# Kernel optimization log

Hardware: AMD Instinct MI355X
Metric: run time of the kernel (lower is better)

Reference implementation:

```python
import jax, jax.numpy as jnp
import numpy as np

# Static config (matches init_kwargs)
B, F, CIN, COUT, H, W = 2, 8, 16, 32, 128, 128
RB, GB = 1, 1                 # refer_band, guard_band_dop (range_doppler)
KH, KW = 2 * (RB + GB), 4     # PeakConv kernel
N = KH * KW                   # ring samples per pixel (16)
LEAK, EPS = 0.01, 1e-5


def _ring_offsets(rb, gb):
    """Peripheral-reference-frame ring offsets, in the exact order of _gen_prf_grid."""
    r = rb + gb
    hp = 2 * r + 1
    xs, ys = np.meshgrid(np.arange(-r, r + 1), np.arange(-r, r + 1), indexing='ij')
    def ring(a):
        top = a[0:rb]
        rgt = a[rb:hp - 2 * rb + 1, hp - rb:hp]
        dwn = a[hp - rb:hp]
        lft = a[rb:hp - 2 * rb + 1, 0:rb]
        return np.concatenate([top.ravel(), rgt.ravel(), dwn.ravel(), lft.ravel()])
    return ring(xs), ring(ys)

_OX, _OY = _ring_offsets(RB, GB)  # each (N,)


def _peak_conv(x, Wk, bk):
    # x: (b, c, h, w)
    bsz, c, h, w = x.shape
    pad = RB + GB
    xp = jnp.pad(x, ((0, 0), (0, 0), (pad, pad), (pad, pad)))
    ii = jnp.arange(h)[:, None, None] + pad + jnp.asarray(_OX)[None, None, :]  # (h,1,N)
    jj = jnp.arange(w)[None, :, None] + pad + jnp.asarray(_OY)[None, None, :]  # (1,w,N)
    x_r = xp[:, :, ii, jj]                       # (b,c,h,w,N) ring gather
    diff = x[..., None] - x_r                    # center minus ring (x_c - x_r)
    diff = diff.reshape(bsz, c, h, w, KH, KW)    # matches _reshape_x_prf tiling
    # conv with kernel (KH,KW), stride (KH,KW) over tiled map == per-pixel contraction
    return jnp.einsum('bchwgj,ocgj->bohw', diff, Wk) + bk[None, :, None, None]


def _bn_leaky(x, gamma, beta):
    mu = x.mean(axis=(0, 2, 3), keepdims=True)
    var = x.var(axis=(0, 2, 3), keepdims=True)  # biased, as torch BN uses for normalization
    y = (x - mu) * jax.lax.rsqrt(var + EPS)
    y = y * gamma[None, :, None, None] + beta[None, :, None, None]
    return jnp.where(y >= 0, y, LEAK * y)


def setup_inputs() -> dict:
    key = jax.random.key(0)
    ks = jax.random.split(key, 5)
    return {
        'x':  jax.random.normal(ks[0], (B, CIN, F, H, W), dtype=jnp.float32),
        'W1': jax.random.normal(ks[1], (COUT, CIN, KH, KW), dtype=jnp.float32) * 0.05,
        'b1': jax.random.normal(ks[2], (COUT,), dtype=jnp.float32) * 0.05,
        'g1': jnp.ones((COUT,), jnp.float32),
        'be1': jnp.zeros((COUT,), jnp.float32),
        'W2': jax.random.normal(ks[3], (COUT, COUT, KH, KW), dtype=jnp.float32) * 0.05,
        'b2': jax.random.normal(ks[4], (COUT,), dtype=jnp.float32) * 0.05,
        'g2': jnp.ones((COUT,), jnp.float32),
        'be2': jnp.zeros((COUT,), jnp.float32),
    }


def reference(x, W1, b1, g1, be1, W2, b2, g2, be2):
    # (B, CIN, F, H, W) -> permute -> flatten to (B*F, CIN, H, W)
    xx = jnp.transpose(x, (0, 2, 1, 3, 4)).reshape(B * F, CIN, H, W)
    y = _bn_leaky(_peak_conv(xx, W1, b1), g1, be1)
    y = _bn_leaky(_peak_conv(y, W2, b2), g2, be2)
    # NOTE: original does .view(B, C, F, h, w) on a (B*F, C, h, w) contiguous
    # tensor — a raw reinterpretation, reproduced exactly by this reshape.
    y = y.reshape(B, COUT, F, H, W)
    return y.mean(axis=2, keepdims=True)  # AvgPool3d((F,1,1)) -> (B, COUT, 1, H, W)
```

## Files before the change

### kernel.cpp

```cpp
#include <hip/hip_runtime.h>
#include <hip/hip_bf16.h>

using short8 = __attribute__((ext_vector_type(8))) short;
using sh4    = __attribute__((ext_vector_type(4))) short;
using f32x4  = __attribute__((ext_vector_type(4))) float;
typedef unsigned short ushort_t;
typedef unsigned long long u64;

constexpr int BB = 2, FF = 8, CIN = 16, COUT = 32, HH = 128, WW = 128;
constexpr int HW   = HH * WW;
constexpr int NIMG = BB * FF;
constexpr int TIL = 16, HALO = 2, LP = 20, NPX = 400;
constexpr int WFN = 17 * 2 * 512;
constexpr int NCPY = 64;
constexpr float FXS  = 65536.f;
constexpr float IFXS = 1.f / 65536.f;

__device__ const int DOFF[17] = { -42,-41,-40,-39,-38, -18,2,22, 38,39,40,41,42, -22,-2,18, 0 };

__device__ __forceinline__ float leaky(float v) { return fmaxf(v, 0.01f * v); }
__device__ __forceinline__ ushort_t f2bf(float f) {
    return __builtin_bit_cast(ushort_t, __float2bfloat16(f));
}
__device__ __forceinline__ float bf2f(ushort_t h) {
    unsigned u = ((unsigned)h) << 16;
    return __builtin_bit_cast(float, u);
}

__device__ __forceinline__ void prm_from_acc(const u64* __restrict__ acc,
                                             const float* __restrict__ gamma,
                                             const float* __restrict__ beta,
                                             float* sprm, int tid)
{
    if (tid < COUT) {
        long long ls = 0, lq = 0;
#pragma unroll
        for (int k = 0; k < NCPY; ++k) {
            ls += (long long)acc[k * 64 + tid];
            lq += (long long)acc[k * 64 + COUT + tid];
        }
        float s = (float)ls * IFXS;
        float q = (float)lq * IFXS;
        const float n = (float)(NIMG * HW);
        float mu  = s / n;
        float var = q / n - mu * mu;
        float a   = gamma[tid] * rsqrtf(var + 1e-5f);
        sprm[tid]        = a;
        sprm[COUT + tid] = beta[tid] - mu * a;
    }
    __syncthreads();
}

template <int MODE>
__device__ __forceinline__ void conv_phase(
    const float* __restrict__ inf, const ushort_t* __restrict__ inh,
    const ushort_t* __restrict__ Wf, const float* __restrict__ bk,
    const float* sprm, ushort_t* __restrict__ tout, u64* __restrict__ acc_g,
    ushort_t* lds, float (*redS)[COUT], float (*redQ)[COUT],
    int img, int tileid, int tid)
{
    const int tx   = (tileid & 7) * TIL;
    const int ty   = (tileid >> 3) * TIL;
    const int lane = tid & 63;
    const int wid  = tid >> 6;
    const int rxl  = lane & 15;
    const int cq   = lane >> 4;

    if (MODE == 0) {
#pragma unroll
        for (int e = 0; e < 4; ++e) {
            int task = e * 256 + tid;
            if (task < 800) {
                int h  = task >= 400 ? 1 : 0;
                int p  = task - h * 400;
                int ry = p / LP, rx = p - ry * LP;
                int gh = ty + ry - HALO, gw = tx + rx - HALO;
                bool ok = (unsigned)gh < (unsigned)HH && (unsigned)gw < (unsigned)WW;
                int ghc = min(max(gh, 0), HH - 1), gwc = min(max(gw, 0), WW - 1);
                const float* base = inf + (((size_t)(img >> 3) * CIN + 8 * h) * FF + (img & 7)) * HW
                                       + ghc * WW + gwc;
                short8 hi8, lo8;
#pragma unroll
                for (int cc = 0; cc < 8; ++cc) {
                    float v = base[(size_t)cc * FF * HW];
                    v = ok ? v : 0.f;
                    ushort_t hi = f2bf(v);
                    hi8[cc] = (short)hi;
                    lo8[cc] = (short)f2bf(v - bf2f(hi));
                }
                int swz = (p & 3) ^ ((p >> 2) & 3);
                *(short8*)&lds[p * 32 + 8 * (h ^ swz)]       = hi8;
                *(short8*)&lds[p * 32 + 8 * ((2 + h) ^ swz)] = lo8;
            }
        }
    } else {
#pragma unroll
        for (int e = 0; e < 7; ++e) {
            int task = e * 256 + tid;
            if (task < 1600) {
                int g  = task & 3, p = task >> 2;
                int ry = p / LP, rx = p - ry * LP;
                int gh = ty + ry - HALO, gw = tx + rx - HALO;
                bool ok = (unsigned)gh < (unsigned)HH && (unsigned)gw < (unsigned)WW;
                int ghc = min(max(gh, 0), HH - 1), gwc = min(max(gw, 0), WW - 1);
                const ushort_t* px = inh + ((size_t)img * HW + ghc * WW + gwc) * 32 + 8 * g;
                short8 raw = *(const short8*)px;
                short8 hv;
#pragma unroll
                for (int jj = 0; jj < 8; ++jj) {
                    int c = 8 * g + jj;
                    float v = bf2f((ushort_t)raw[jj]);
                    v = leaky(fmaf(sprm[c], v, sprm[COUT + c]));
                    hv[jj] = (short)f2bf(ok ? v : 0.f);
                }
                int swz = (p & 3) ^ ((p >> 2) & 3);
                *(short8*)&lds[p * 32 + 8 * (g ^ swz)] = hv;
            }
        }
    }
    __syncthreads();

    f32x4 acc[4][2];
#pragma unroll
    for (int ng = 0; ng < 4; ++ng)
#pragma unroll
        for (int oh = 0; oh < 2; ++oh) acc[ng][oh] = f32x4{0.f, 0.f, 0.f, 0.f};

    int q0[4];
#pragma unroll
    for (int ng = 0; ng < 4; ++ng) q0[ng] = (wid * 4 + ng + HALO) * LP + (rxl + HALO);

    const ushort_t* wl = Wf + (size_t)lane * 8;

#pragma unroll
    for (int n = 0; n < 17; ++n) {
        short8 A0 = *(const short8*)(wl + (size_t)(n * 2 + 0) * 512);
        short8 A1 = *(const short8*)(wl + (size_t)(n * 2 + 1) * 512);
        int dof = DOFF[n];
#pragma unroll
        for (int ng = 0; ng < 4; ++ng) {
            int p   = q0[ng] + dof;
            int swz = (p & 3) ^ ((p >> 2) & 3);
            short8 Bv = *(const short8*)&lds[p * 32 + 8 * (cq ^ swz)];
            acc[ng][0] = __builtin_amdgcn_mfma_f32_16x16x32_bf16(A0, Bv, acc[ng][0], 0, 0, 0);
            acc[ng][1] = __builtin_amdgcn_mfma_f32_16x16x32_bf16(A1, Bv, acc[ng][1], 0, 0, 0);
        }
    }

    float ssum[2][4], ssq[2][4];
#pragma unroll
    for (int oh = 0; oh < 2; ++oh)
#pragma unroll
        for (int rr = 0; rr < 4; ++rr) {
            float b = bk[oh * 16 + cq * 4 + rr];
#pragma unroll
            for (int ng = 0; ng < 4; ++ng) acc[ng][oh][rr] += b;
            ssum[oh][rr] = 0.f; ssq[oh][rr] = 0.f;
        }

#pragma unroll
    for (int ng = 0; ng < 4; ++ng) {
        int gh = ty + wid * 4 + ng, gw = tx + rxl;
        size_t pxb = ((size_t)img * HW + gh * WW + gw) * 32;
#pragma unroll
        for (int oh = 0; oh < 2; ++oh) {
            sh4 sv;
#pragma unroll
            for (int rr = 0; rr < 4; ++rr) {
                float v = acc[ng][oh][rr];
                sv[rr] = (short)f2bf(v);
                ssum[oh][rr] += v;
                ssq[oh][rr]   = fmaf(v, v, ssq[oh][rr]);
            }
            *(sh4*)&tout[pxb + oh * 16 + cq * 4] = sv;
        }
    }

#pragma unroll
    for (int oh = 0; oh < 2; ++oh)
#pragma unroll
        for (int rr = 0; rr < 4; ++rr) {
            float s = ssum[oh][rr], q = ssq[oh][rr];
#pragma unroll
            for (int m = 1; m < 16; m <<= 1) { s += __shfl_xor(s, m); q += __shfl_xor(q, m); }
            if (rxl == 0) {
                redS[wid][oh * 16 + cq * 4 + rr] = s;
                redQ[wid][oh * 16 + cq * 4 + rr] = q;
            }
        }
    __syncthreads();

    if (tid < COUT) {
        float s = redS[0][tid] + redS[1][tid] + redS[2][tid] + redS[3][tid];
        float q = redQ[0][tid] + redQ[1][tid] + redQ[2][tid] + redQ[3][tid];
        long long qs = (long long)llrintf(s * FXS);
        long long qq = (long long)llrintf(q * FXS);
        int copy = (img * 64 + tileid) & (NCPY - 1);
        atomicAdd(&acc_g[copy * 64 + tid],        (u64)qs);
        atomicAdd(&acc_g[copy * 64 + COUT + tid], (u64)qq);
    }
}

__global__ __launch_bounds__(256)
void prep_weights(const float* __restrict__ W1, const float* __restrict__ W2,
                  ushort_t* __restrict__ Wf1, ushort_t* __restrict__ Wf2,
                  u64* __restrict__ accz)
{
    if (blockIdx.y == 0 && blockIdx.x < (2 * NCPY * 64) / 256) {
        accz[blockIdx.x * 256 + threadIdx.x] = 0ull;
    }
    int which = blockIdx.y;
    const float* W = which ? W2 : W1;
    ushort_t* Wf   = which ? Wf2 : Wf1;
    int ci         = which ? COUT : CIN;
    int idx = blockIdx.x * 256 + threadIdx.x;
    int j  = idx & 7;
    int l  = (idx >> 3) & 63;
    int oh = (idx >> 9) & 1;
    int n  = idx >> 10;
    int oc = oh * 16 + (l & 15);
    int k  = ((l >> 4) << 3) + j;
    int c  = which ? k : (k & 15);
    const float* wp = W + ((size_t)oc * ci + c) * 16;
    float v;
    if (n < 16) v = -wp[n];
    else { v = 0.f; for (int q = 0; q < 16; ++q) v += wp[q]; }
    Wf[idx] = f2bf(v);
}

__global__ __launch_bounds__(256)
void conv1_k(const float* __restrict__ x, const ushort_t* __restrict__ Wf1,
             const float* __restrict__ b1, ushort_t* __restrict__ t1,
             u64* __restrict__ acc1)
{
    __shared__ __align__(16) ushort_t lds[NPX * 32];
    __shared__ float redS[4][COUT], redQ[4][COUT];
    conv_phase<0>(x, nullptr, Wf1, b1, nullptr, t1, acc1,
                  lds, redS, redQ, blockIdx.y, blockIdx.x, threadIdx.x);
}

__global__ __launch_bounds__(256)
void conv2_k(const ushort_t* __restrict__ t1, const ushort_t* __restrict__ Wf2,
             const float* __restrict__ b2, const u64* __restrict__ acc1,
             const float* __restrict__ g1, const float* __restrict__ be1,
             ushort_t* __restrict__ t2, u64* __restrict__ acc2)
{
    __shared__ __align__(16) ushort_t lds[NPX * 32];
    __shared__ float redS[4][COUT], redQ[4][COUT];
    __shared__ float sprm[2 * COUT];
    prm_from_acc(acc1, g1, be1, sprm, threadIdx.x);
    conv_phase<1>(nullptr, t1, Wf2, b2, sprm, t2, acc2,
                  lds, redS, redQ, blockIdx.y, blockIdx.x, threadIdx.x);
}

__global__ __launch_bounds__(256)
void finalize_k(const ushort_t* __restrict__ t2, const u64* __restrict__ acc2,
                const float* __restrict__ g2, const float* __restrict__ be2,
                float* __restrict__ outp)
{
    __shared__ float sprm[2 * COUT];
    prm_from_acc(acc2, g2, be2, sprm, threadIdx.x);
    int base = blockIdx.x * 4096;
#pragma unroll
    for (int e = 0; e < 16; ++e) {
        int gid  = base + e * 256 + threadIdx.x;
        int p    = gid & (HW - 1);
        int rest = gid >> 14;
        int o    = rest & 31;
        int b    = rest >> 5;
        int img  = b * 8 + (o >> 2);
        int cb   = (o & 3) * 8;
        const ushort_t* px = t2 + ((size_t)img * HW + p) * 32 + cb;
        short8 raw = *(const short8*)px;
        float s = 0.f;
#pragma unroll
        for (int j = 0; j < 8; ++j) {
            int c = cb + j;
            float v = bf2f((ushort_t)raw[j]);
            s += leaky(fmaf(sprm[c], v, sprm[COUT + c]));
        }
        outp[gid] = 0.125f * s;
    }
}

extern "C" void kernel_launch(void* const* d_in, const int* in_sizes, int n_in,
                              void* d_out, int out_size, void* d_ws, size_t ws_size,
                              hipStream_t stream)
{
    const float* x   = (const float*)d_in[0];
    const float* W1  = (const float*)d_in[1];
    const float* b1  = (const float*)d_in[2];
    const float* g1  = (const float*)d_in[3];
    const float* be1 = (const float*)d_in[4];
    const float* W2  = (const float*)d_in[5];
    const float* b2  = (const float*)d_in[6];
    const float* g2  = (const float*)d_in[7];
    const float* be2 = (const float*)d_in[8];
    float* out = (float*)d_out;

    const size_t TSZH = (size_t)NIMG * HW * 32;
    ushort_t* t1   = (ushort_t*)d_ws;
    ushort_t* t2   = t1 + TSZH;
    u64*      acc1 = (u64*)(t2 + TSZH);
    u64*      acc2 = acc1 + NCPY * 64;
    ushort_t* Wf1  = (ushort_t*)(acc2 + NCPY * 64);
    ushort_t* Wf2  = Wf1 + WFN;

    dim3 pg(WFN / 256, 2);
    prep_weights<<<pg, 256, 0, stream>>>(W1, W2, Wf1, Wf2, acc1);
    dim3 cg_(64, NIMG);
    conv1_k<<<cg_, 256, 0, stream>>>(x, Wf1, b1, t1, acc1);
    conv2_k<<<cg_, 256, 0, stream>>>(t1, Wf2, b2, acc1, g1, be1, t2, acc2);
    finalize_k<<<(BB * COUT * HW) / 4096, 256, 0, stream>>>(t2, acc2, g2, be2, out);
}
```

Before: 61.30 us.

## Process two tiles per block with register-staged prefetch overlapping compute

```diff
diff --git a/kernel.cpp b/kernel.cpp
--- a/kernel.cpp
+++ b/kernel.cpp
@@ -51,12 +51,102 @@
     __syncthreads();
 }
 
-template <int MODE>
-__device__ __forceinline__ void conv_phase(
-    const float* __restrict__ inf, const ushort_t* __restrict__ inh,
-    const ushort_t* __restrict__ Wf, const float* __restrict__ bk,
-    const float* sprm, ushort_t* __restrict__ tout, u64* __restrict__ acc_g,
-    ushort_t* lds, float (*redS)[COUT], float (*redQ)[COUT],
+struct Regs0 { float v[4][8]; };
+struct Regs1 { short8 v[7]; };
+
+__device__ __forceinline__ void load0(Regs0& r, const float* __restrict__ inf,
+                                      int img, int tileid, int tid)
+{
+    const int tx = (tileid & 7) * TIL, ty = (tileid >> 3) * TIL;
+#pragma unroll
+    for (int e = 0; e < 4; ++e) {
+        int task = min(e * 256 + tid, 799);
+        int h  = task >= 400 ? 1 : 0;
+        int p  = task - h * 400;
+        int ry = p / LP, rx = p - ry * LP;
+        int gh = ty + ry - HALO, gw = tx + rx - HALO;
+        int ghc = min(max(gh, 0), HH - 1), gwc = min(max(gw, 0), WW - 1);
+        const float* base = inf + (((size_t)(img >> 3) * CIN + 8 * h) * FF + (img & 7)) * HW
+                               + ghc * WW + gwc;
+#pragma unroll
+        for (int cc = 0; cc < 8; ++cc) r.v[e][cc] = base[(size_t)cc * FF * HW];
+    }
+}
+
+__device__ __forceinline__ void write0(const Regs0& r, ushort_t* lds,
+                                       int img, int tileid, int tid)
+{
+    const int tx = (tileid & 7) * TIL, ty = (tileid >> 3) * TIL;
+#pragma unroll
+    for (int e = 0; e < 4; ++e) {
+        int task = e * 256 + tid;
+        if (task < 800) {
+            int h  = task >= 400 ? 1 : 0;
+            int p  = task - h * 400;
+            int ry = p / LP, rx = p - ry * LP;
+            int gh = ty + ry - HALO, gw = tx + rx - HALO;
+            bool ok = (unsigned)gh < (unsigned)HH && (unsigned)gw < (unsigned)WW;
+            short8 hi8, lo8;
+#pragma unroll
+            for (int cc = 0; cc < 8; ++cc) {
+                float v = ok ? r.v[e][cc] : 0.f;
+                ushort_t hi = f2bf(v);
+                hi8[cc] = (short)hi;
+                lo8[cc] = (short)f2bf(v - bf2f(hi));
+            }
+            int swz = (p & 3) ^ ((p >> 2) & 3);
+            *(short8*)&lds[p * 32 + 8 * (h ^ swz)]       = hi8;
+            *(short8*)&lds[p * 32 + 8 * ((2 + h) ^ swz)] = lo8;
+        }
+    }
+}
+
+__device__ __forceinline__ void load1(Regs1& r, const ushort_t* __restrict__ inh,
+                                      int img, int tileid, int tid)
+{
+    const int tx = (tileid & 7) * TIL, ty = (tileid >> 3) * TIL;
+#pragma unroll
+    for (int e = 0; e < 7; ++e) {
+        int task = min(e * 256 + tid, 1599);
+        int g  = task & 3, p = task >> 2;
+        int ry = p / LP, rx = p - ry * LP;
+        int gh = ty + ry - HALO, gw = tx + rx - HALO;
+        int ghc = min(max(gh, 0), HH - 1), gwc = min(max(gw, 0), WW - 1);
+        r.v[e] = *(const short8*)(inh + ((size_t)img * HW + ghc * WW + gwc) * 32 + 8 * g);
+    }
+}
+
+__device__ __forceinline__ void write1(const Regs1& r, ushort_t* lds, const float* sprm,
+                                       int img, int tileid, int tid)
+{
+    const int tx = (tileid & 7) * TIL, ty = (tileid >> 3) * TIL;
+#pragma unroll
+    for (int e = 0; e < 7; ++e) {
+        int task = e * 256 + tid;
+        if (task < 1600) {
+            int g  = task & 3, p = task >> 2;
+            int ry = p / LP, rx = p - ry * LP;
+            int gh = ty + ry - HALO, gw = tx + rx - HALO;
+            bool ok = (unsigned)gh < (unsigned)HH && (unsigned)gw < (unsigned)WW;
+            short8 raw = r.v[e];
+            short8 hv;
+#pragma unroll
+            for (int jj = 0; jj < 8; ++jj) {
+                int c = 8 * g + jj;
+                float v = bf2f((ushort_t)raw[jj]);
+                v = leaky(fmaf(sprm[c], v, sprm[COUT + c]));
+                hv[jj] = (short)f2bf(ok ? v : 0.f);
+            }
+            int swz = (p & 3) ^ ((p >> 2) & 3);
+            *(short8*)&lds[p * 32 + 8 * (g ^ swz)] = hv;
+        }
+    }
+}
+
+__device__ __forceinline__ void compute_pre(
+    const ushort_t* lds, const ushort_t* __restrict__ Wf,
+    const float* __restrict__ bk, ushort_t* __restrict__ tout,
+    float (*redS)[COUT], float (*redQ)[COUT],
     int img, int tileid, int tid)
 {
     const int tx   = (tileid & 7) * TIL;
@@ -65,60 +155,6 @@
     const int wid  = tid >> 6;
     const int rxl  = lane & 15;
     const int cq   = lane >> 4;
-
-    if (MODE == 0) {
-#pragma unroll
-        for (int e = 0; e < 4; ++e) {
-            int task = e * 256 + tid;
-            if (task < 800) {
-                int h  = task >= 400 ? 1 : 0;
-                int p  = task - h * 400;
-                int ry = p / LP, rx = p - ry * LP;
-                int gh = ty + ry - HALO, gw = tx + rx - HALO;
-                bool ok = (unsigned)gh < (unsigned)HH && (unsigned)gw < (unsigned)WW;
-                int ghc = min(max(gh, 0), HH - 1), gwc = min(max(gw, 0), WW - 1);
-                const float* base = inf + (((size_t)(img >> 3) * CIN + 8 * h) * FF + (img & 7)) * HW
-                                       + ghc * WW + gwc;
-                short8 hi8, lo8;
-#pragma unroll
-                for (int cc = 0; cc < 8; ++cc) {
-                    float v = base[(size_t)cc * FF * HW];
-                    v = ok ? v : 0.f;
-                    ushort_t hi = f2bf(v);
-                    hi8[cc] = (short)hi;
-                    lo8[cc] = (short)f2bf(v - bf2f(hi));
-                }
-                int swz = (p & 3) ^ ((p >> 2) & 3);
-                *(short8*)&lds[p * 32 + 8 * (h ^ swz)]       = hi8;
-                *(short8*)&lds[p * 32 + 8 * ((2 + h) ^ swz)] = lo8;
-            }
-        }
-    } else {
-#pragma unroll
-        for (int e = 0; e < 7; ++e) {
-            int task = e * 256 + tid;
-            if (task < 1600) {
-                int g  = task & 3, p = task >> 2;
-                int ry = p / LP, rx = p - ry * LP;
-                int gh = ty + ry - HALO, gw = tx + rx - HALO;
-                bool ok = (unsigned)gh < (unsigned)HH && (unsigned)gw < (unsigned)WW;
-                int ghc = min(max(gh, 0), HH - 1), gwc = min(max(gw, 0), WW - 1);
-                const ushort_t* px = inh + ((size_t)img * HW + ghc * WW + gwc) * 32 + 8 * g;
-                short8 raw = *(const short8*)px;
-                short8 hv;
-#pragma unroll
-                for (int jj = 0; jj < 8; ++jj) {
-                    int c = 8 * g + jj;
-                    float v = bf2f((ushort_t)raw[jj]);
-                    v = leaky(fmaf(sprm[c], v, sprm[COUT + c]));
-                    hv[jj] = (short)f2bf(ok ? v : 0.f);
-                }
-                int swz = (p & 3) ^ ((p >> 2) & 3);
-                *(short8*)&lds[p * 32 + 8 * (g ^ swz)] = hv;
-            }
-        }
-    }
-    __syncthreads();
 
     f32x4 acc[4][2];
 #pragma unroll
@@ -188,8 +224,11 @@
                 redQ[wid][oh * 16 + cq * 4 + rr] = q;
             }
         }
-    __syncthreads();
-
+}
+
+__device__ __forceinline__ void post_atomic(const float (*redS)[COUT], const float (*redQ)[COUT],
+                                            u64* __restrict__ acc_g, int img, int tileid, int tid)
+{
     if (tid < COUT) {
         float s = redS[0][tid] + redS[1][tid] + redS[2][tid] + redS[3][tid];
         float q = redQ[0][tid] + redQ[1][tid] + redQ[2][tid] + redQ[3][tid];
@@ -228,29 +267,57 @@
     Wf[idx] = f2bf(v);
 }
 
-__global__ __launch_bounds__(256)
+__global__ __launch_bounds__(256, 2)
 void conv1_k(const float* __restrict__ x, const ushort_t* __restrict__ Wf1,
              const float* __restrict__ b1, ushort_t* __restrict__ t1,
              u64* __restrict__ acc1)
 {
-    __shared__ __align__(16) ushort_t lds[NPX * 32];
-    __shared__ float redS[4][COUT], redQ[4][COUT];
-    conv_phase<0>(x, nullptr, Wf1, b1, nullptr, t1, acc1,
-                  lds, redS, redQ, blockIdx.y, blockIdx.x, threadIdx.x);
-}
-
-__global__ __launch_bounds__(256)
+    __shared__ __align__(16) ushort_t lds[2][NPX * 32];
+    __shared__ float redS[2][4][COUT], redQ[2][4][COUT];
+    const int tid = threadIdx.x;
+    const int ta = blockIdx.x * 2, tb = ta + 1;
+    const int imga = ta >> 6, tida = ta & 63;
+    const int imgb = tb >> 6, tidb = tb & 63;
+
+    Regs0 rA; load0(rA, x, imga, tida, tid);
+    write0(rA, lds[0], imga, tida, tid);
+    Regs0 rB; load0(rB, x, imgb, tidb, tid);
+    __syncthreads();
+    compute_pre(lds[0], Wf1, b1, t1, redS[0], redQ[0], imga, tida, tid);
+    write0(rB, lds[1], imgb, tidb, tid);
+    __syncthreads();
+    post_atomic(redS[0], redQ[0], acc1, imga, tida, tid);
+    compute_pre(lds[1], Wf1, b1, t1, redS[1], redQ[1], imgb, tidb, tid);
+    __syncthreads();
+    post_atomic(redS[1], redQ[1], acc1, imgb, tidb, tid);
+}
+
+__global__ __launch_bounds__(256, 2)
 void conv2_k(const ushort_t* __restrict__ t1, const ushort_t* __restrict__ Wf2,
              const float* __restrict__ b2, const u64* __restrict__ acc1,
              const float* __restrict__ g1, const float* __restrict__ be1,
              ushort_t* __restrict__ t2, u64* __restrict__ acc2)
 {
-    __shared__ __align__(16) ushort_t lds[NPX * 32];
-    __shared__ float redS[4][COUT], redQ[4][COUT];
+    __shared__ __align__(16) ushort_t lds[2][NPX * 32];
+    __shared__ float redS[2][4][COUT], redQ[2][4][COUT];
     __shared__ float sprm[2 * COUT];
-    prm_from_acc(acc1, g1, be1, sprm, threadIdx.x);
-    conv_phase<1>(nullptr, t1, Wf2, b2, sprm, t2, acc2,
-                  lds, redS, redQ, blockIdx.y, blockIdx.x, threadIdx.x);
+    const int tid = threadIdx.x;
+    const int ta = blockIdx.x * 2, tb = ta + 1;
+    const int imga = ta >> 6, tida = ta & 63;
+    const int imgb = tb >> 6, tidb = tb & 63;
+
+    prm_from_acc(acc1, g1, be1, sprm, tid);
+    Regs1 rA; load1(rA, t1, imga, tida, tid);
+    write1(rA, lds[0], sprm, imga, tida, tid);
+    Regs1 rB; load1(rB, t1, imgb, tidb, tid);
+    __syncthreads();
+    compute_pre(lds[0], Wf2, b2, t2, redS[0], redQ[0], imga, tida, tid);
+    write1(rB, lds[1], sprm, imgb, tidb, tid);
+    __syncthreads();
+    post_atomic(redS[0], redQ[0], acc2, imga, tida, tid);
+    compute_pre(lds[1], Wf2, b2, t2, redS[1], redQ[1], imgb, tidb, tid);
+    __syncthreads();
+    post_atomic(redS[1], redQ[1], acc2, imgb, tidb, tid);
 }
 
 __global__ __launch_bounds__(256)
@@ -308,8 +375,7 @@
 
     dim3 pg(WFN / 256, 2);
     prep_weights<<<pg, 256, 0, stream>>>(W1, W2, Wf1, Wf2, acc1);
-    dim3 cg_(64, NIMG);
-    conv1_k<<<cg_, 256, 0, stream>>>(x, Wf1, b1, t1, acc1);
-    conv2_k<<<cg_, 256, 0, stream>>>(t1, Wf2, b2, acc1, g1, be1, t2, acc2);
+    conv1_k<<<512, 256, 0, stream>>>(x, Wf1, b1, t1, acc1);
+    conv2_k<<<512, 256, 0, stream>>>(t1, Wf2, b2, acc1, g1, be1, t2, acc2);
     finalize_k<<<(BB * COUT * HW) / 4096, 256, 0, stream>>>(t2, acc2, g2, be2, out);
 }
```

Result: slower. 64.87 us (+5.8%).

## Split BN1 apply into padded buffer pass; conv2 reads operands directly from global

Applied to the files above, without the earlier changes.

```diff
diff --git a/kernel.cpp b/kernel.cpp
--- a/kernel.cpp
+++ b/kernel.cpp
@@ -11,12 +11,16 @@
 constexpr int HW   = HH * WW;
 constexpr int NIMG = BB * FF;
 constexpr int TIL = 16, HALO = 2, LP = 20, NPX = 400;
+constexpr int PW  = 132;
+constexpr int NRING = PW * PW - HH * WW;
 constexpr int WFN = 17 * 2 * 512;
 constexpr int NCPY = 64;
 constexpr float FXS  = 65536.f;
 constexpr float IFXS = 1.f / 65536.f;
 
 __device__ const int DOFF[17] = { -42,-41,-40,-39,-38, -18,2,22, 38,39,40,41,42, -22,-2,18, 0 };
+__device__ const int D2[17] = { -8512,-8480,-8448,-8416,-8384, -4160,64,4288,
+                                 8384,8416,8448,8480,8512, -4288,-64,4160, 0 };
 
 __device__ __forceinline__ float leaky(float v) { return fmaxf(v, 0.01f * v); }
 __device__ __forceinline__ ushort_t f2bf(float f) {
@@ -51,169 +55,28 @@
     __syncthreads();
 }
 
-template <int MODE>
-__device__ __forceinline__ void conv_phase(
-    const float* __restrict__ inf, const ushort_t* __restrict__ inh,
-    const ushort_t* __restrict__ Wf, const float* __restrict__ bk,
-    const float* sprm, ushort_t* __restrict__ tout, u64* __restrict__ acc_g,
-    ushort_t* lds, float (*redS)[COUT], float (*redQ)[COUT],
-    int img, int tileid, int tid)
-{
-    const int tx   = (tileid & 7) * TIL;
-    const int ty   = (tileid >> 3) * TIL;
-    const int lane = tid & 63;
-    const int wid  = tid >> 6;
-    const int rxl  = lane & 15;
-    const int cq   = lane >> 4;
-
-    if (MODE == 0) {
-#pragma unroll
-        for (int e = 0; e < 4; ++e) {
-            int task = e * 256 + tid;
-            if (task < 800) {
-                int h  = task >= 400 ? 1 : 0;
-                int p  = task - h * 400;
-                int ry = p / LP, rx = p - ry * LP;
-                int gh = ty + ry - HALO, gw = tx + rx - HALO;
-                bool ok = (unsigned)gh < (unsigned)HH && (unsigned)gw < (unsigned)WW;
-                int ghc = min(max(gh, 0), HH - 1), gwc = min(max(gw, 0), WW - 1);
-                const float* base = inf + (((size_t)(img >> 3) * CIN + 8 * h) * FF + (img & 7)) * HW
-                                       + ghc * WW + gwc;
-                short8 hi8, lo8;
-#pragma unroll
-                for (int cc = 0; cc < 8; ++cc) {
-                    float v = base[(size_t)cc * FF * HW];
-                    v = ok ? v : 0.f;
-                    ushort_t hi = f2bf(v);
-                    hi8[cc] = (short)hi;
-                    lo8[cc] = (short)f2bf(v - bf2f(hi));
-                }
-                int swz = (p & 3) ^ ((p >> 2) & 3);
-                *(short8*)&lds[p * 32 + 8 * (h ^ swz)]       = hi8;
-                *(short8*)&lds[p * 32 + 8 * ((2 + h) ^ swz)] = lo8;
-            }
-        }
-    } else {
-#pragma unroll
-        for (int e = 0; e < 7; ++e) {
-            int task = e * 256 + tid;
-            if (task < 1600) {
-                int g  = task & 3, p = task >> 2;
-                int ry = p / LP, rx = p - ry * LP;
-                int gh = ty + ry - HALO, gw = tx + rx - HALO;
-                bool ok = (unsigned)gh < (unsigned)HH && (unsigned)gw < (unsigned)WW;
-                int ghc = min(max(gh, 0), HH - 1), gwc = min(max(gw, 0), WW - 1);
-                const ushort_t* px = inh + ((size_t)img * HW + ghc * WW + gwc) * 32 + 8 * g;
-                short8 raw = *(const short8*)px;
-                short8 hv;
-#pragma unroll
-                for (int jj = 0; jj < 8; ++jj) {
-                    int c = 8 * g + jj;
-                    float v = bf2f((ushort_t)raw[jj]);
-                    v = leaky(fmaf(sprm[c], v, sprm[COUT + c]));
-                    hv[jj] = (short)f2bf(ok ? v : 0.f);
-                }
-                int swz = (p & 3) ^ ((p >> 2) & 3);
-                *(short8*)&lds[p * 32 + 8 * (g ^ swz)] = hv;
-            }
-        }
-    }
-    __syncthreads();
-
-    f32x4 acc[4][2];
-#pragma unroll
-    for (int ng = 0; ng < 4; ++ng)
-#pragma unroll
-        for (int oh = 0; oh < 2; ++oh) acc[ng][oh] = f32x4{0.f, 0.f, 0.f, 0.f};
-
-    int q0[4];
-#pragma unroll
-    for (int ng = 0; ng < 4; ++ng) q0[ng] = (wid * 4 + ng + HALO) * LP + (rxl + HALO);
-
-    const ushort_t* wl = Wf + (size_t)lane * 8;
-
-#pragma unroll
-    for (int n = 0; n < 17; ++n) {
-        short8 A0 = *(const short8*)(wl + (size_t)(n * 2 + 0) * 512);
-        short8 A1 = *(const short8*)(wl + (size_t)(n * 2 + 1) * 512);
-        int dof = DOFF[n];
-#pragma unroll
-        for (int ng = 0; ng < 4; ++ng) {
-            int p   = q0[ng] + dof;
-            int swz = (p & 3) ^ ((p >> 2) & 3);
-            short8 Bv = *(const short8*)&lds[p * 32 + 8 * (cq ^ swz)];
-            acc[ng][0] = __builtin_amdgcn_mfma_f32_16x16x32_bf16(A0, Bv, acc[ng][0], 0, 0, 0);
-            acc[ng][1] = __builtin_amdgcn_mfma_f32_16x16x32_bf16(A1, Bv, acc[ng][1], 0, 0, 0);
-        }
-    }
-
-    float ssum[2][4], ssq[2][4];
-#pragma unroll
-    for (int oh = 0; oh < 2; ++oh)
-#pragma unroll
-        for (int rr = 0; rr < 4; ++rr) {
-            float b = bk[oh * 16 + cq * 4 + rr];
-#pragma unroll
-            for (int ng = 0; ng < 4; ++ng) acc[ng][oh][rr] += b;
-            ssum[oh][rr] = 0.f; ssq[oh][rr] = 0.f;
-        }
-
-#pragma unroll
-    for (int ng = 0; ng < 4; ++ng) {
-        int gh = ty + wid * 4 + ng, gw = tx + rxl;
-        size_t pxb = ((size_t)img * HW + gh * WW + gw) * 32;
-#pragma unroll
-        for (int oh = 0; oh < 2; ++oh) {
-            sh4 sv;
-#pragma unroll
-            for (int rr = 0; rr < 4; ++rr) {
-                float v = acc[ng][oh][rr];
-                sv[rr] = (short)f2bf(v);
-                ssum[oh][rr] += v;
-                ssq[oh][rr]   = fmaf(v, v, ssq[oh][rr]);
-            }
-            *(sh4*)&tout[pxb + oh * 16 + cq * 4] = sv;
-        }
-    }
-
-#pragma unroll
-    for (int oh = 0; oh < 2; ++oh)
-#pragma unroll
-        for (int rr = 0; rr < 4; ++rr) {
-            float s = ssum[oh][rr], q = ssq[oh][rr];
-#pragma unroll
-            for (int m = 1; m < 16; m <<= 1) { s += __shfl_xor(s, m); q += __shfl_xor(q, m); }
-            if (rxl == 0) {
-                redS[wid][oh * 16 + cq * 4 + rr] = s;
-                redQ[wid][oh * 16 + cq * 4 + rr] = q;
-            }
-        }
-    __syncthreads();
-
-    if (tid < COUT) {
-        float s = redS[0][tid] + redS[1][tid] + redS[2][tid] + redS[3][tid];
-        float q = redQ[0][tid] + redQ[1][tid] + redQ[2][tid] + redQ[3][tid];
-        long long qs = (long long)llrintf(s * FXS);
-        long long qq = (long long)llrintf(q * FXS);
-        int copy = (img * 64 + tileid) & (NCPY - 1);
-        atomicAdd(&acc_g[copy * 64 + tid],        (u64)qs);
-        atomicAdd(&acc_g[copy * 64 + COUT + tid], (u64)qq);
-    }
-}
-
 __global__ __launch_bounds__(256)
 void prep_weights(const float* __restrict__ W1, const float* __restrict__ W2,
                   ushort_t* __restrict__ Wf1, ushort_t* __restrict__ Wf2,
-                  u64* __restrict__ accz)
-{
-    if (blockIdx.y == 0 && blockIdx.x < (2 * NCPY * 64) / 256) {
-        accz[blockIdx.x * 256 + threadIdx.x] = 0ull;
+                  u64* __restrict__ accz, ushort_t* __restrict__ t1p)
+{
+    int idx = blockIdx.x * 256 + threadIdx.x;
+    if (blockIdx.y == 0) {
+        if (blockIdx.x < (2 * NCPY * 64) / 256) accz[idx] = 0ull;
+        if (idx < NIMG * NRING) {
+            int img = idx / NRING, r = idx - img * NRING;
+            int row, col;
+            if (r < 528) { int rr = r / 132; row = rr < 2 ? rr : rr + 128; col = r % 132; }
+            else { int q = r - 528; row = 2 + (q >> 2); int c4 = q & 3; col = c4 < 2 ? c4 : c4 + 128; }
+            f32x4* dst = (f32x4*)(t1p + ((size_t)(img * PW + row) * PW + col) * 32);
+            f32x4 z = {0.f, 0.f, 0.f, 0.f};
+            dst[0] = z; dst[1] = z; dst[2] = z; dst[3] = z;
+        }
     }
     int which = blockIdx.y;
     const float* W = which ? W2 : W1;
     ushort_t* Wf   = which ? Wf2 : Wf1;
     int ci         = which ? COUT : CIN;
-    int idx = blockIdx.x * 256 + threadIdx.x;
     int j  = idx & 7;
     int l  = (idx >> 3) & 63;
     int oh = (idx >> 9) & 1;
@@ -229,28 +92,247 @@
 }
 
 __global__ __launch_bounds__(256)
-void conv1_k(const float* __restrict__ x, const ushort_t* __restrict__ Wf1,
-             const float* __restrict__ b1, ushort_t* __restrict__ t1,
-             u64* __restrict__ acc1)
+void conv1_k(const float* __restrict__ inf, const ushort_t* __restrict__ Wf,
+             const float* __restrict__ bk, ushort_t* __restrict__ tout,
+             u64* __restrict__ acc_g)
 {
     __shared__ __align__(16) ushort_t lds[NPX * 32];
     __shared__ float redS[4][COUT], redQ[4][COUT];
-    conv_phase<0>(x, nullptr, Wf1, b1, nullptr, t1, acc1,
-                  lds, redS, redQ, blockIdx.y, blockIdx.x, threadIdx.x);
+    const int tid = threadIdx.x, tileid = blockIdx.x, img = blockIdx.y;
+    const int tx   = (tileid & 7) * TIL;
+    const int ty   = (tileid >> 3) * TIL;
+    const int lane = tid & 63;
+    const int wid  = tid >> 6;
+    const int rxl  = lane & 15;
+    const int cq   = lane >> 4;
+
+#pragma unroll
+    for (int e = 0; e < 4; ++e) {
+        int task = e * 256 + tid;
+        if (task < 800) {
+            int h  = task >= 400 ? 1 : 0;
+            int p  = task - h * 400;
+            int ry = p / LP, rx = p - ry * LP;
+            int gh = ty + ry - HALO, gw = tx + rx - HALO;
+            bool ok = (unsigned)gh < (unsigned)HH && (unsigned)gw < (unsigned)WW;
+            int ghc = min(max(gh, 0), HH - 1), gwc = min(max(gw, 0), WW - 1);
+            const float* base = inf + (((size_t)(img >> 3) * CIN + 8 * h) * FF + (img & 7)) * HW
+                                   + ghc * WW + gwc;
+            short8 hi8, lo8;
+#pragma unroll
+            for (int cc = 0; cc < 8; ++cc) {
+                float v = base[(size_t)cc * FF * HW];
+                v = ok ? v : 0.f;
+                ushort_t hi = f2bf(v);
+                hi8[cc] = (short)hi;
+                lo8[cc] = (short)f2bf(v - bf2f(hi));
+            }
+            int swz = (p & 3) ^ ((p >> 2) & 3);
+            *(short8*)&lds[p * 32 + 8 * (h ^ swz)]       = hi8;
+            *(short8*)&lds[p * 32 + 8 * ((2 + h) ^ swz)] = lo8;
+        }
+    }
+    __syncthreads();
+
+    f32x4 acc[4][2];
+#pragma unroll
+    for (int ng = 0; ng < 4; ++ng)
+#pragma unroll
+        for (int oh = 0; oh < 2; ++oh) acc[ng][oh] = f32x4{0.f, 0.f, 0.f, 0.f};
+
+    int q0[4];
+#pragma unroll
+    for (int ng = 0; ng < 4; ++ng) q0[ng] = (wid * 4 + ng + HALO) * LP + (rxl + HALO);
+
+    const ushort_t* wl = Wf + (size_t)lane * 8;
+
+#pragma unroll
+    for (int n = 0; n < 17; ++n) {
+        short8 A0 = *(const short8*)(wl + (size_t)(n * 2 + 0) * 512);
+        short8 A1 = *(const short8*)(wl + (size_t)(n * 2 + 1) * 512);
+        int dof = DOFF[n];
+#pragma unroll
+        for (int ng = 0; ng < 4; ++ng) {
+            int p   = q0[ng] + dof;
+            int swz = (p & 3) ^ ((p >> 2) & 3);
+            short8 Bv = *(const short8*)&lds[p * 32 + 8 * (cq ^ swz)];
+            acc[ng][0] = __builtin_amdgcn_mfma_f32_16x16x32_bf16(A0, Bv, acc[ng][0], 0, 0, 0);
+            acc[ng][1] = __builtin_amdgcn_mfma_f32_16x16x32_bf16(A1, Bv, acc[ng][1], 0, 0, 0);
+        }
+    }
+
+    float ssum[2][4], ssq[2][4];
+#pragma unroll
+    for (int oh = 0; oh < 2; ++oh)
+#pragma unroll
+        for (int rr = 0; rr < 4; ++rr) {
+            float b = bk[oh * 16 + cq * 4 + rr];
+#pragma unroll
+            for (int ng = 0; ng < 4; ++ng) acc[ng][oh][rr] += b;
+            ssum[oh][rr] = 0.f; ssq[oh][rr] = 0.f;
+        }
+
+#pragma unroll
+    for (int ng = 0; ng < 4; ++ng) {
+        int gh = ty + wid * 4 + ng, gw = tx + rxl;
+        size_t pxb = ((size_t)img * HW + gh * WW + gw) * 32;
+#pragma unroll
+        for (int oh = 0; oh < 2; ++oh) {
+            sh4 sv;
+#pragma unroll
+            for (int rr = 0; rr < 4; ++rr) {
+                float v = acc[ng][oh][rr];
+                sv[rr] = (short)f2bf(v);
+                ssum[oh][rr] += v;
+                ssq[oh][rr]   = fmaf(v, v, ssq[oh][rr]);
+            }
+            *(sh4*)&tout[pxb + oh * 16 + cq * 4] = sv;
+        }
+    }
+
+#pragma unroll
+    for (int oh = 0; oh < 2; ++oh)
+#pragma unroll
+        for (int rr = 0; rr < 4; ++rr) {
+            float s = ssum[oh][rr], q = ssq[oh][rr];
+#pragma unroll
+            for (int m = 1; m < 16; m <<= 1) { s += __shfl_xor(s, m); q += __shfl_xor(q, m); }
+            if (rxl == 0) {
+                redS[wid][oh * 16 + cq * 4 + rr] = s;
+                redQ[wid][oh * 16 + cq * 4 + rr] = q;
+            }
+        }
+    __syncthreads();
+
+    if (tid < COUT) {
+        float s = redS[0][tid] + redS[1][tid] + redS[2][tid] + redS[3][tid];
+        float q = redQ[0][tid] + redQ[1][tid] + redQ[2][tid] + redQ[3][tid];
+        long long qs = (long long)llrintf(s * FXS);
+        long long qq = (long long)llrintf(q * FXS);
+        int copy = (img * 64 + tileid) & (NCPY - 1);
+        atomicAdd(&acc_g[copy * 64 + tid],        (u64)qs);
+        atomicAdd(&acc_g[copy * 64 + COUT + tid], (u64)qq);
+    }
 }
 
 __global__ __launch_bounds__(256)
-void conv2_k(const ushort_t* __restrict__ t1, const ushort_t* __restrict__ Wf2,
-             const float* __restrict__ b2, const u64* __restrict__ acc1,
+void bnapply(const ushort_t* __restrict__ t1, const u64* __restrict__ acc1,
              const float* __restrict__ g1, const float* __restrict__ be1,
-             ushort_t* __restrict__ t2, u64* __restrict__ acc2)
-{
-    __shared__ __align__(16) ushort_t lds[NPX * 32];
-    __shared__ float redS[4][COUT], redQ[4][COUT];
+             ushort_t* __restrict__ t1p)
+{
     __shared__ float sprm[2 * COUT];
     prm_from_acc(acc1, g1, be1, sprm, threadIdx.x);
-    conv_phase<1>(nullptr, t1, Wf2, b2, sprm, t2, acc2,
-                  lds, redS, redQ, blockIdx.y, blockIdx.x, threadIdx.x);
+#pragma unroll
+    for (int e = 0; e < 4; ++e) {
+        int task = blockIdx.x * 1024 + e * 256 + threadIdx.x;
+        int g   = task & 3;
+        int p   = (task >> 2) & (HW - 1);
+        int img = task >> 16;
+        short8 raw = *(const short8*)(t1 + ((size_t)img * HW + p) * 32 + 8 * g);
+        short8 hv;
+#pragma unroll
+        for (int jj = 0; jj < 8; ++jj) {
+            int c = 8 * g + jj;
+            float v = bf2f((ushort_t)raw[jj]);
+            hv[jj] = (short)f2bf(leaky(fmaf(sprm[c], v, sprm[COUT + c])));
+        }
+        int row = (p >> 7) + 2, col = (p & 127) + 2;
+        *(short8*)(t1p + ((size_t)(img * PW + row) * PW + col) * 32 + 8 * g) = hv;
+    }
+}
+
+__global__ __launch_bounds__(256)
+void conv2_k(const ushort_t* __restrict__ t1p, const ushort_t* __restrict__ Wf,
+             const float* __restrict__ bk, ushort_t* __restrict__ tout,
+             u64* __restrict__ acc_g)
+{
+    __shared__ float redS[4][COUT], redQ[4][COUT];
+    const int tid = threadIdx.x, tileid = blockIdx.x, img = blockIdx.y;
+    const int tx   = (tileid & 7) * TIL;
+    const int ty   = (tileid >> 3) * TIL;
+    const int lane = tid & 63;
+    const int wid  = tid >> 6;
+    const int rxl  = lane & 15;
+    const int cq   = lane >> 4;
+
+    f32x4 acc[4][2];
+#pragma unroll
+    for (int ng = 0; ng < 4; ++ng)
+#pragma unroll
+        for (int oh = 0; oh < 2; ++oh) acc[ng][oh] = f32x4{0.f, 0.f, 0.f, 0.f};
+
+    const ushort_t* bp[4];
+#pragma unroll
+    for (int ng = 0; ng < 4; ++ng)
+        bp[ng] = t1p + ((size_t)(img * PW + ty + wid * 4 + ng + 2) * PW + tx + rxl + 2) * 32 + cq * 8;
+
+    const ushort_t* wl = Wf + (size_t)lane * 8;
+
+#pragma unroll
+    for (int n = 0; n < 17; ++n) {
+        short8 A0 = *(const short8*)(wl + (size_t)(n * 2 + 0) * 512);
+        short8 A1 = *(const short8*)(wl + (size_t)(n * 2 + 1) * 512);
+        int d = D2[n];
+#pragma unroll
+        for (int ng = 0; ng < 4; ++ng) {
+            short8 Bv = *(const short8*)(bp[ng] + d);
+            acc[ng][0] = __builtin_amdgcn_mfma_f32_16x16x32_bf16(A0, Bv, acc[ng][0], 0, 0, 0);
+            acc[ng][1] = __builtin_amdgcn_mfma_f32_16x16x32_bf16(A1, Bv, acc[ng][1], 0, 0, 0);
+        }
+    }
+
+    float ssum[2][4], ssq[2][4];
+#pragma unroll
+    for (int oh = 0; oh < 2; ++oh)
+#pragma unroll
+        for (int rr = 0; rr < 4; ++rr) {
+            float b = bk[oh * 16 + cq * 4 + rr];
+#pragma unroll
+            for (int ng = 0; ng < 4; ++ng) acc[ng][oh][rr] += b;
+            ssum[oh][rr] = 0.f; ssq[oh][rr] = 0.f;
+        }
+
+#pragma unroll
+    for (int ng = 0; ng < 4; ++ng) {
+        int gh = ty + wid * 4 + ng, gw = tx + rxl;
+        size_t pxb = ((size_t)img * HW + gh * WW + gw) * 32;
+#pragma unroll
+        for (int oh = 0; oh < 2; ++oh) {
+            sh4 sv;
+#pragma unroll
+            for (int rr = 0; rr < 4; ++rr) {
+                float v = acc[ng][oh][rr];
+                sv[rr] = (short)f2bf(v);
+                ssum[oh][rr] += v;
+                ssq[oh][rr]   = fmaf(v, v, ssq[oh][rr]);
+            }
+            *(sh4*)&tout[pxb + oh * 16 + cq * 4] = sv;
+        }
+    }
+
+#pragma unroll
+    for (int oh = 0; oh < 2; ++oh)
+#pragma unroll
+        for (int rr = 0; rr < 4; ++rr) {
+            float s = ssum[oh][rr], q = ssq[oh][rr];
+#pragma unroll
+            for (int m = 1; m < 16; m <<= 1) { s += __shfl_xor(s, m); q += __shfl_xor(q, m); }
+            if (rxl == 0) {
+                redS[wid][oh * 16 + cq * 4 + rr] = s;
+                redQ[wid][oh * 16 + cq * 4 + rr] = q;
+            }
+        }
+    __syncthreads();
+
+    if (tid < COUT) {
+        float s = redS[0][tid] + redS[1][tid] + redS[2][tid] + redS[3][tid];
+        float q = redQ[0][tid] + redQ[1][tid] + redQ[2][tid] + redQ[3][tid];
+        long long qs = (long long)llrintf(s * FXS);
+        long long qq = (long long)llrintf(q * FXS);
+        int copy = (img * 64 + tileid) & (NCPY - 1);
+        atomicAdd(&acc_g[copy * 64 + tid],        (u64)qs);
+        atomicAdd(&acc_g[copy * 64 + COUT + tid], (u64)qq);
+    }
 }
 
 __global__ __launch_bounds__(256)
@@ -299,17 +381,20 @@
     float* out = (float*)d_out;
 
     const size_t TSZH = (size_t)NIMG * HW * 32;
+    const size_t TPSZ = (size_t)NIMG * PW * PW * 32;
     ushort_t* t1   = (ushort_t*)d_ws;
     ushort_t* t2   = t1 + TSZH;
-    u64*      acc1 = (u64*)(t2 + TSZH);
+    ushort_t* t1p  = t2 + TSZH;
+    u64*      acc1 = (u64*)(t1p + TPSZ);
     u64*      acc2 = acc1 + NCPY * 64;
     ushort_t* Wf1  = (ushort_t*)(acc2 + NCPY * 64);
     ushort_t* Wf2  = Wf1 + WFN;
 
     dim3 pg(WFN / 256, 2);
-    prep_weights<<<pg, 256, 0, stream>>>(W1, W2, Wf1, Wf2, acc1);
+    prep_weights<<<pg, 256, 0, stream>>>(W1, W2, Wf1, Wf2, acc1, t1p);
     dim3 cg_(64, NIMG);
     conv1_k<<<cg_, 256, 0, stream>>>(x, Wf1, b1, t1, acc1);
-    conv2_k<<<cg_, 256, 0, stream>>>(t1, Wf2, b2, acc1, g1, be1, t2, acc2);
+    bnapply<<<1024, 256, 0, stream>>>(t1, acc1, g1, be1, t1p);
+    conv2_k<<<cg_, 256, 0, stream>>>(t1p, Wf2, b2, t2, acc2);
     finalize_k<<<(BB * COUT * HW) / 4096, 256, 0, stream>>>(t2, acc2, g2, be2, out);
 }
```

Result: slower. 77.28 us (+26.1%).
